# Kernel tuning notes

Hardware: AMD Instinct MI355X
Metric: run time of the kernel (lower is better)

## Reference

```python
import math
import jax, jax.numpy as jnp
import numpy as np

D_MODEL = 1024
N_HEADS = 16
D_HEAD = D_MODEL // N_HEADS


def setup_inputs() -> dict:
    key = jax.random.key(0)
    kx, kqkv, ko = jax.random.split(key, 3)
    B, T = 4, 2048
    x = jax.random.normal(kx, (B, T, D_MODEL), dtype=jnp.float32)
    # Linear(d_model, 3*d_model, bias=False): weight stored as [out, in]
    s = 1.0 / math.sqrt(D_MODEL)
    W_qkv = jax.random.uniform(kqkv, (3 * D_MODEL, D_MODEL), dtype=jnp.float32, minval=-s, maxval=s)
    W_o = jax.random.uniform(ko, (D_MODEL, D_MODEL), dtype=jnp.float32, minval=-s, maxval=s)
    return {"x": x, "W_qkv": W_qkv, "W_o": W_o}


def reference(x, W_qkv, W_o):
    B, T, C = x.shape
    H, Dh = N_HEADS, D_HEAD
    qkv = jnp.einsum('btc,oc->bto', x, W_qkv)            # [B,T,3C]
    qkv = qkv.reshape(B, T, 3, H, Dh)
    q = jnp.transpose(qkv[:, :, 0], (0, 2, 1, 3))        # [B,H,T,Dh]
    k = jnp.transpose(qkv[:, :, 1], (0, 2, 1, 3))
    v = jnp.transpose(qkv[:, :, 2], (0, 2, 1, 3))
    scale = 1.0 / math.sqrt(Dh)
    attn = jnp.einsum('bhqd,bhkd->bhqk', q, k) * scale   # [B,H,T,T]
    causal = jnp.tril(jnp.ones((T, T), dtype=bool))
    attn = jnp.where(causal, attn, -jnp.inf)
    attn = jax.nn.softmax(attn, axis=-1)
    out = jnp.einsum('bhqk,bhkd->bhqd', attn, v)         # [B,H,T,Dh]
    out = jnp.transpose(out, (0, 2, 1, 3)).reshape(B, T, C)
    return jnp.einsum('btc,oc->bto', out, W_o)
```

## Files before the change

kernel.cpp:

```cpp
#include <hip/hip_runtime.h>
#include <hip/hip_bf16.h>
#include <cstdint>

#define TT      2048
#define NBATCH  4
#define BTROWS  8192
#define CDIM    1024
#define NQKV    3072
#define QSCALE  0.18033688011112042f

using bf16x8 = __attribute__((ext_vector_type(8))) short;
using f32x4  = __attribute__((ext_vector_type(4))) float;
using f32x16 = __attribute__((ext_vector_type(16))) float;

#define GLOAD_LDS16(g, l)                                                     \
  __builtin_amdgcn_global_load_lds(                                           \
      (const __attribute__((address_space(1))) unsigned int*)(g),             \
      (__attribute__((address_space(3))) unsigned int*)(l), 16, 0, 0)

__device__ inline short f2bf(float f) {
  unsigned u = __builtin_bit_cast(unsigned, f);
  u += 0x7FFF + ((u >> 16) & 1);
  return (short)(u >> 16);
}

__global__ __launch_bounds__(256) void conv_bf16(const float* __restrict__ in,
                                                 short* __restrict__ out, int n) {
  int i = (blockIdx.x * 256 + threadIdx.x) * 4;
  if (i + 3 < n) {
    float4 v = *(const float4*)(in + i);
    short4 o;
    o.x = f2bf(v.x); o.y = f2bf(v.y); o.z = f2bf(v.z); o.w = f2bf(v.w);
    *(short4*)(out + i) = o;
  }
}

__global__ __launch_bounds__(256) void gemm_qkv(const short* __restrict__ A,
                                                const short* __restrict__ Bw,
                                                short* __restrict__ Qb,
                                                short* __restrict__ Kb,
                                                short* __restrict__ Vb) {
  const int K = CDIM;
  __shared__ __attribute__((aligned(16))) short smem[8192];
  short* As = smem;
  short* Bs = smem + 4096;
  int tid = threadIdx.x;
  int bid = blockIdx.x;
  int bm = ((bid & 7) << 3) | (bid >> 3);
  int bn = blockIdx.y;
  int lane = tid & 63, wid = tid >> 6;
  int wr = wid >> 1, wc = wid & 1;
  int la = lane & 15, lg = lane >> 4;

  const short* Ab = A + (size_t)bm * 128 * K;
  const short* Bb = Bw + (size_t)bn * 128 * K;

  f32x4 acc[4][4];
#pragma unroll
  for (int m = 0; m < 4; m++)
#pragma unroll
    for (int n = 0; n < 4; n++) acc[m][n] = (f32x4){0.f, 0.f, 0.f, 0.f};

  int c0 = tid, c1 = tid + 256;
  for (int k0 = 0; k0 < K; k0 += 32) {
    GLOAD_LDS16(Ab + (c0 >> 2) * K + k0 + (c0 & 3) * 8, &As[c0 * 8]);
    GLOAD_LDS16(Ab + (c1 >> 2) * K + k0 + (c1 & 3) * 8, &As[c1 * 8]);
    GLOAD_LDS16(Bb + (c0 >> 2) * K + k0 + (c0 & 3) * 8, &Bs[c0 * 8]);
    GLOAD_LDS16(Bb + (c1 >> 2) * K + k0 + (c1 & 3) * 8, &Bs[c1 * 8]);
    __syncthreads();
    bf16x8 af[4], bfr[4];
#pragma unroll
    for (int m = 0; m < 4; m++)
      af[m] = *(const bf16x8*)&As[(wr * 64 + m * 16 + la) * 32 + lg * 8];
#pragma unroll
    for (int n = 0; n < 4; n++)
      bfr[n] = *(const bf16x8*)&Bs[(wc * 64 + n * 16 + la) * 32 + lg * 8];
#pragma unroll
    for (int m = 0; m < 4; m++)
#pragma unroll
      for (int n = 0; n < 4; n++)
        acc[m][n] = __builtin_amdgcn_mfma_f32_16x16x32_bf16(af[m], bfr[n],
                                                            acc[m][n], 0, 0, 0);
    __syncthreads();
  }

  int colbase = bn * 128 + wc * 64;
  int which = colbase >> 10;
  int b = bm >> 4;

  if (which == 2) {
#pragma unroll
    for (int m = 0; m < 4; m++) {
      int tb = (bm * 128 + wr * 64 + m * 16 + lg * 4) & 2047;
#pragma unroll
      for (int n = 0; n < 4; n++) {
        int col = colbase + n * 16 + la;
        int h = (col >> 6) & 15;
        int d = col & 63;
        short4 o4;
        o4.x = f2bf(acc[m][n][0]); o4.y = f2bf(acc[m][n][1]);
        o4.z = f2bf(acc[m][n][2]); o4.w = f2bf(acc[m][n][3]);
        *(short4*)&Vb[((size_t)(b * 16 + h) * 64 + d) * TT + tb] = o4;
      }
    }
  } else {
    short* dst = (which == 0) ? Qb : Kb;
    float sc = (which == 0) ? QSCALE : 1.0f;
    int h = (colbase >> 6) & 15;
    size_t hbase = ((size_t)(b * 16 + h) * TT) * 64;
    short* Ls = smem + wid * (16 * 72);
    int rrow = lane & 15, chunk = lane >> 4;
#pragma unroll
    for (int m = 0; m < 4; m++) {
#pragma unroll
      for (int n = 0; n < 4; n++)
#pragma unroll
        for (int r = 0; r < 4; r++)
          Ls[(lg * 4 + r) * 72 + n * 16 + la] = f2bf(acc[m][n][r] * sc);
      __syncthreads();
      int t = (bm * 128 + wr * 64 + m * 16 + rrow) & 2047;
      bf16x8 v0 = *(const bf16x8*)&Ls[rrow * 72 + chunk * 16];
      bf16x8 v1 = *(const bf16x8*)&Ls[rrow * 72 + chunk * 16 + 8];
      *(bf16x8*)&dst[hbase + (size_t)t * 64 + chunk * 16] = v0;
      *(bf16x8*)&dst[hbase + (size_t)t * 64 + chunk * 16 + 8] = v1;
      __syncthreads();
    }
  }
}

__global__ __launch_bounds__(256, 3) void attn_fwd2(const short* __restrict__ Qb,
                                                    const short* __restrict__ Kb,
                                                    const short* __restrict__ Vtg,
                                                    short* __restrict__ Ob) {
  __shared__ __attribute__((aligned(16))) short lds[10240];
  short* Ks = lds;
  short* Vs = lds + 4096;

  int tid = threadIdx.x, lane = tid & 63, w = tid >> 6;
  int l31 = lane & 31, hi = lane >> 5, l7 = lane & 7;
  int gid = blockIdx.x;
  int qt = 15 - (gid & 15);
  int bh = gid >> 4;
  int q0 = qt * 128;
  int qw = q0 + w * 32;
  int qg = qw + l31;

  const short* Qh = Qb + (size_t)bh * TT * 64;
  const short* Kh = Kb + (size_t)bh * TT * 64;
  const short* Vh = Vtg + (size_t)bh * 64 * TT;

  bf16x8 q[4];
#pragma unroll
  for (int c = 0; c < 4; c++)
    q[c] = *(const bf16x8*)(Qh + (size_t)qg * 64 + c * 16 + hi * 8);

  f32x16 o0, o1;
#pragma unroll
  for (int r = 0; r < 16; r++) { o0[r] = 0.f; o1[r] = 0.f; }
  float m = -1e30f, lsum = 0.f;

  int nt = 2 * qt + 2;
  int c0 = tid, c1 = tid + 256;
  int r0 = c0 >> 3, cc0 = c0 & 7;
  int r1 = c1 >> 3, cc1 = c1 & 7;

  bf16x8 kr0, kr1, vr0, vr1;
  kr0 = *(const bf16x8*)(Kh + (size_t)r0 * 64 + cc0 * 8);
  kr1 = *(const bf16x8*)(Kh + (size_t)r1 * 64 + cc1 * 8);
  vr0 = *(const bf16x8*)(Vh + (size_t)r0 * TT + cc0 * 8);
  vr1 = *(const bf16x8*)(Vh + (size_t)r1 * TT + cc1 * 8);

  for (int it = 0; it < nt; it++) {
    int kv0 = it * 64;
    __syncthreads();
    *(bf16x8*)&Ks[r0 * 64 + ((cc0 ^ (r0 & 7)) * 8)] = kr0;
    *(bf16x8*)&Ks[r1 * 64 + ((cc1 ^ (r1 & 7)) * 8)] = kr1;
    *(bf16x8*)&Vs[r0 * 64 + ((cc0 ^ (r0 & 7)) * 8)] = vr0;
    *(bf16x8*)&Vs[r1 * 64 + ((cc1 ^ (r1 & 7)) * 8)] = vr1;
    __syncthreads();
    if (it + 1 < nt) {
      int kn = kv0 + 64;
      kr0 = *(const bf16x8*)(Kh + (size_t)(kn + r0) * 64 + cc0 * 8);
      kr1 = *(const bf16x8*)(Kh + (size_t)(kn + r1) * 64 + cc1 * 8);
      vr0 = *(const bf16x8*)(Vh + (size_t)r0 * TT + kn + cc0 * 8);
      vr1 = *(const bf16x8*)(Vh + (size_t)r1 * TT + kn + cc1 * 8);
    }
    if (kv0 <= qw + 31) {
      f32x16 st0, st1;
#pragma unroll
      for (int r = 0; r < 16; r++) { st0[r] = 0.f; st1[r] = 0.f; }
      __builtin_amdgcn_s_setprio(1);
#pragma unroll
      for (int c = 0; c < 4; c++) {
        int cc = c * 2 + hi;
        bf16x8 kf0 = *(const bf16x8*)&Ks[l31 * 64 + ((cc ^ l7) * 8)];
        bf16x8 kf1 = *(const bf16x8*)&Ks[(32 + l31) * 64 + ((cc ^ l7) * 8)];
        st0 = __builtin_amdgcn_mfma_f32_32x32x16_bf16(kf0, q[c], st0, 0, 0, 0);
        st1 = __builtin_amdgcn_mfma_f32_32x32x16_bf16(kf1, q[c], st1, 0, 0, 0);
      }
      __builtin_amdgcn_s_setprio(0);
      if (kv0 + 63 > qw) {
#pragma unroll
        for (int r = 0; r < 16; r++) {
          int kloc = (r & 3) + 8 * (r >> 2) + 4 * hi;
          if (kv0 + kloc > qg)      st0[r] = -1e30f;
          if (kv0 + 32 + kloc > qg) st1[r] = -1e30f;
        }
      }
      float tm[16];
#pragma unroll
      for (int r = 0; r < 16; r++) tm[r] = fmaxf(st0[r], st1[r]);
#pragma unroll
      for (int s = 8; s >= 1; s >>= 1)
#pragma unroll
        for (int r = 0; r < 16; r++)
          if (r < s) tm[r] = fmaxf(tm[r], tm[r + s]);
      float pm = tm[0];
      pm = fmaxf(pm, __shfl_xor(pm, 32));
      if (!__all(pm <= m + 8.f)) {
        float mn = fmaxf(m, pm);
        float fac = exp2f(m - mn);
        lsum *= fac;
#pragma unroll
        for (int r = 0; r < 16; r++) { o0[r] *= fac; o1[r] *= fac; }
        m = mn;
      }
      float ts[16];
#pragma unroll
      for (int r = 0; r < 16; r++) {
        st0[r] = exp2f(st0[r] - m);
        st1[r] = exp2f(st1[r] - m);
        ts[r] = st0[r] + st1[r];
      }
#pragma unroll
      for (int s = 8; s >= 1; s >>= 1)
#pragma unroll
        for (int r = 0; r < 16; r++)
          if (r < s) ts[r] += ts[r + s];
      float rs = ts[0];
      rs += __shfl_xor(rs, 32);
      lsum += rs;
      __builtin_amdgcn_s_setprio(1);
#pragma unroll
      for (int kb = 0; kb < 2; kb++) {
#pragma unroll
        for (int c2 = 0; c2 < 2; c2++) {
          float p0 = kb ? st1[8 * c2 + 0] : st0[8 * c2 + 0];
          float p1 = kb ? st1[8 * c2 + 1] : st0[8 * c2 + 1];
          float p2 = kb ? st1[8 * c2 + 2] : st0[8 * c2 + 2];
          float p3 = kb ? st1[8 * c2 + 3] : st0[8 * c2 + 3];
          float p4 = kb ? st1[8 * c2 + 4] : st0[8 * c2 + 4];
          float p5 = kb ? st1[8 * c2 + 5] : st0[8 * c2 + 5];
          float p6 = kb ? st1[8 * c2 + 6] : st0[8 * c2 + 6];
          float p7 = kb ? st1[8 * c2 + 7] : st0[8 * c2 + 7];
          unsigned u0, u1, u2, u3;
          asm("v_cvt_pk_bf16_f32 %0, %1, %2" : "=v"(u0) : "v"(p0), "v"(p1));
          asm("v_cvt_pk_bf16_f32 %0, %1, %2" : "=v"(u1) : "v"(p2), "v"(p3));
          asm("v_cvt_pk_bf16_f32 %0, %1, %2" : "=v"(u2) : "v"(p4), "v"(p5));
          asm("v_cvt_pk_bf16_f32 %0, %1, %2" : "=v"(u3) : "v"(p6), "v"(p7));
          asm volatile("v_permlane32_swap_b32 %0, %1" : "+v"(u0), "+v"(u2));
          asm volatile("v_permlane32_swap_b32 %0, %1" : "+v"(u1), "+v"(u3));
          union { unsigned u[4]; bf16x8 v; } pa;
          pa.u[0] = u0; pa.u[1] = u1; pa.u[2] = u2; pa.u[3] = u3;
          int ccv = kb * 4 + c2 * 2 + hi;
          bf16x8 vf0 = *(const bf16x8*)&Vs[l31 * 64 + ((ccv ^ l7) * 8)];
          bf16x8 vf1 = *(const bf16x8*)&Vs[(32 + l31) * 64 + ((ccv ^ l7) * 8)];
          o0 = __builtin_amdgcn_mfma_f32_32x32x16_bf16(vf0, pa.v, o0, 0, 0, 0);
          o1 = __builtin_amdgcn_mfma_f32_32x32x16_bf16(vf1, pa.v, o1, 0, 0, 0);
        }
      }
      __builtin_amdgcn_s_setprio(0);
    }
  }

  __syncthreads();
  short* Os = lds + w * (32 * 80);
  float inv = 1.f / lsum;
#pragma unroll
  for (int k = 0; k < 4; k++) {
    float a0 = o0[4 * k + 0] * inv, a1 = o0[4 * k + 1] * inv;
    float a2 = o0[4 * k + 2] * inv, a3 = o0[4 * k + 3] * inv;
    float b0 = o1[4 * k + 0] * inv, b1 = o1[4 * k + 1] * inv;
    float b2 = o1[4 * k + 2] * inv, b3 = o1[4 * k + 3] * inv;
    unsigned w0, w1, w2, w3;
    asm("v_cvt_pk_bf16_f32 %0, %1, %2" : "=v"(w0) : "v"(a0), "v"(a1));
    asm("v_cvt_pk_bf16_f32 %0, %1, %2" : "=v"(w1) : "v"(a2), "v"(a3));
    asm("v_cvt_pk_bf16_f32 %0, %1, %2" : "=v"(w2) : "v"(b0), "v"(b1));
    asm("v_cvt_pk_bf16_f32 %0, %1, %2" : "=v"(w3) : "v"(b2), "v"(b3));
    int d = 8 * k + 4 * hi;
    uint2 pa; pa.x = w0; pa.y = w1;
    uint2 pb; pb.x = w2; pb.y = w3;
    *(uint2*)&Os[l31 * 80 + d] = pa;
    *(uint2*)&Os[l31 * 80 + 32 + d] = pb;
  }
  __syncthreads();
  int b = bh >> 4, h = bh & 15;
#pragma unroll
  for (int pass = 0; pass < 4; pass++) {
    int qr = pass * 8 + (lane >> 3);
    int cc = lane & 7;
    bf16x8 v = *(const bf16x8*)&Os[qr * 80 + cc * 8];
    *(bf16x8*)&Ob[((size_t)(b * TT + q0 + w * 32 + qr)) * CDIM + h * 64 + cc * 8] = v;
  }
}

__global__ __launch_bounds__(256) void gemm_out(const short* __restrict__ A,
                                                const short* __restrict__ Bw,
                                                float* __restrict__ C) {
  const int K = CDIM;
  __shared__ __attribute__((aligned(16))) short As[128 * 32];
  __shared__ __attribute__((aligned(16))) short Bs[128 * 32];
  int tid = threadIdx.x;
  int bid = blockIdx.x;
  int bm = ((bid & 7) << 3) | (bid >> 3);
  int bn = blockIdx.y;
  int lane = tid & 63, wid = tid >> 6;
  int wr = wid >> 1, wc = wid & 1;
  int la = lane & 15, lg = lane >> 4;

  const short* Ab = A + (size_t)bm * 128 * K;
  const short* Bb = Bw + (size_t)bn * 128 * K;

  f32x4 acc[4][4];
#pragma unroll
  for (int m = 0; m < 4; m++)
#pragma unroll
    for (int n = 0; n < 4; n++) acc[m][n] = (f32x4){0.f, 0.f, 0.f, 0.f};

  int c0 = tid, c1 = tid + 256;
  for (int k0 = 0; k0 < K; k0 += 32) {
    GLOAD_LDS16(Ab + (c0 >> 2) * K + k0 + (c0 & 3) * 8, &As[c0 * 8]);
    GLOAD_LDS16(Ab + (c1 >> 2) * K + k0 + (c1 & 3) * 8, &As[c1 * 8]);
    GLOAD_LDS16(Bb + (c0 >> 2) * K + k0 + (c0 & 3) * 8, &Bs[c0 * 8]);
    GLOAD_LDS16(Bb + (c1 >> 2) * K + k0 + (c1 & 3) * 8, &Bs[c1 * 8]);
    __syncthreads();
    bf16x8 af[4], bfr[4];
#pragma unroll
    for (int m = 0; m < 4; m++)
      af[m] = *(const bf16x8*)&As[(wr * 64 + m * 16 + la) * 32 + lg * 8];
#pragma unroll
    for (int n = 0; n < 4; n++)
      bfr[n] = *(const bf16x8*)&Bs[(wc * 64 + n * 16 + la) * 32 + lg * 8];
#pragma unroll
    for (int m = 0; m < 4; m++)
#pragma unroll
      for (int n = 0; n < 4; n++)
        acc[m][n] = __builtin_amdgcn_mfma_f32_16x16x32_bf16(af[m], bfr[n],
                                                            acc[m][n], 0, 0, 0);
    __syncthreads();
  }

#pragma unroll
  for (int m = 0; m < 4; m++) {
    int rbase = bm * 128 + wr * 64 + m * 16 + lg * 4;
#pragma unroll
    for (int n = 0; n < 4; n++) {
      int col = bn * 128 + wc * 64 + n * 16 + la;
#pragma unroll
      for (int r = 0; r < 4; r++)
        C[(size_t)(rbase + r) * CDIM + col] = acc[m][n][r];
    }
  }
}

extern "C" void kernel_launch(void* const* d_in, const int* in_sizes, int n_in,
                              void* d_out, int out_size, void* d_ws, size_t ws_size,
                              hipStream_t stream) {
  const float* x    = (const float*)d_in[0];
  const float* wqkv = (const float*)d_in[1];
  const float* wo   = (const float*)d_in[2];
  float* out = (float*)d_out;

  char* ws = (char*)d_ws;
  short* xb  = (short*)(ws);
  short* wqb = (short*)(ws + (size_t)(16 << 20));
  short* wob = (short*)(ws + (size_t)(22 << 20));
  short* Qb  = (short*)(ws + (size_t)(24 << 20));
  short* Kb  = (short*)(ws + (size_t)(40 << 20));
  short* Vb  = (short*)(ws + (size_t)(56 << 20));
  short* Ob  = (short*)(ws + (size_t)(72 << 20));

  conv_bf16<<<8192, 256, 0, stream>>>(x, xb, BTROWS * CDIM);
  conv_bf16<<<3072, 256, 0, stream>>>(wqkv, wqb, NQKV * CDIM);
  conv_bf16<<<1024, 256, 0, stream>>>(wo, wob, CDIM * CDIM);

  gemm_qkv<<<dim3(BTROWS / 128, NQKV / 128), 256, 0, stream>>>(xb, wqb, Qb, Kb, Vb);
  attn_fwd2<<<NBATCH * 16 * (TT / 128), 256, 0, stream>>>(Qb, Kb, Vb, Ob);
  gemm_out<<<dim3(BTROWS / 128, CDIM / 128), 256, 0, stream>>>(Ob, wob, out);
}
```

Before: 308.2 us.

## Double-buffer attention K/V tiles with direct global-to-LDS async loads

The attention kernel previously loaded the next K/V tile into registers and then stored it into shared memory, which took two barriers per iteration. It now issues global_load_lds copies straight into a double-buffered shared-memory region, prefetching tile it+1 while tile it is being computed. This removes the register staging, the explicit LDS stores and one barrier per iteration. In exchange, shared memory per block grows from 20KB to 32KB, and correctness depends on the async LDS writes being complete before the barrier.

```diff
diff --git a/kernel.cpp b/kernel.cpp
--- a/kernel.cpp
+++ b/kernel.cpp
@@ -132,9 +132,7 @@
                                                     const short* __restrict__ Kb,
                                                     const short* __restrict__ Vtg,
                                                     short* __restrict__ Ob) {
-  __shared__ __attribute__((aligned(16))) short lds[10240];
-  short* Ks = lds;
-  short* Vs = lds + 4096;
+  __shared__ __attribute__((aligned(16))) short lds[16384];
 
   int tid = threadIdx.x, lane = tid & 63, w = tid >> 6;
   int l31 = lane & 31, hi = lane >> 5, l7 = lane & 7;
@@ -160,32 +158,28 @@
   float m = -1e30f, lsum = 0.f;
 
   int nt = 2 * qt + 2;
-  int c0 = tid, c1 = tid + 256;
-  int r0 = c0 >> 3, cc0 = c0 & 7;
-  int r1 = c1 >> 3, cc1 = c1 & 7;
-
-  bf16x8 kr0, kr1, vr0, vr1;
-  kr0 = *(const bf16x8*)(Kh + (size_t)r0 * 64 + cc0 * 8);
-  kr1 = *(const bf16x8*)(Kh + (size_t)r1 * 64 + cc1 * 8);
-  vr0 = *(const bf16x8*)(Vh + (size_t)r0 * TT + cc0 * 8);
-  vr1 = *(const bf16x8*)(Vh + (size_t)r1 * TT + cc1 * 8);
-
+  int s0 = w * 128 + lane, s1 = s0 + 64;
+  int r0 = s0 >> 3, sc0 = (s0 & 7) ^ (r0 & 7);
+  int r1 = s1 >> 3, sc1 = (s1 & 7) ^ (r1 & 7);
+
+#define STAGE_KV(b, kv0s)                                                     \
+  {                                                                           \
+    short* KB = lds + (b) * 8192;                                             \
+    short* VB = KB + 4096;                                                    \
+    GLOAD_LDS16(Kh + (size_t)((kv0s) + r0) * 64 + sc0 * 8, &KB[s0 * 8]);      \
+    GLOAD_LDS16(Kh + (size_t)((kv0s) + r1) * 64 + sc1 * 8, &KB[s1 * 8]);      \
+    GLOAD_LDS16(Vh + (size_t)r0 * TT + (kv0s) + sc0 * 8, &VB[s0 * 8]);        \
+    GLOAD_LDS16(Vh + (size_t)r1 * TT + (kv0s) + sc1 * 8, &VB[s1 * 8]);        \
+  }
+
+  STAGE_KV(0, 0);
   for (int it = 0; it < nt; it++) {
     int kv0 = it * 64;
     __syncthreads();
-    *(bf16x8*)&Ks[r0 * 64 + ((cc0 ^ (r0 & 7)) * 8)] = kr0;
-    *(bf16x8*)&Ks[r1 * 64 + ((cc1 ^ (r1 & 7)) * 8)] = kr1;
-    *(bf16x8*)&Vs[r0 * 64 + ((cc0 ^ (r0 & 7)) * 8)] = vr0;
-    *(bf16x8*)&Vs[r1 * 64 + ((cc1 ^ (r1 & 7)) * 8)] = vr1;
-    __syncthreads();
-    if (it + 1 < nt) {
-      int kn = kv0 + 64;
-      kr0 = *(const bf16x8*)(Kh + (size_t)(kn + r0) * 64 + cc0 * 8);
-      kr1 = *(const bf16x8*)(Kh + (size_t)(kn + r1) * 64 + cc1 * 8);
-      vr0 = *(const bf16x8*)(Vh + (size_t)r0 * TT + kn + cc0 * 8);
-      vr1 = *(const bf16x8*)(Vh + (size_t)r1 * TT + kn + cc1 * 8);
-    }
+    if (it + 1 < nt) STAGE_KV((it + 1) & 1, kv0 + 64);
     if (kv0 <= qw + 31) {
+      short* Ks = lds + (it & 1) * 8192;
+      short* Vs = Ks + 4096;
       f32x16 st0, st1;
 #pragma unroll
       for (int r = 0; r < 16; r++) { st0[r] = 0.f; st1[r] = 0.f; }
```

New measurement: 311.9 us. Within noise of the previous version (+1.2%).
